# Optimization experiments

Hardware: AMD Instinct MI355X
Metric: run time of the kernel (lower is better)

Reference implementation:

```python
import jax, jax.numpy as jnp
import numpy as np

N_NODES = 100000
N_FEATS = 256
OUT_DIM = 64
NNZ_X = 1280000
N_EDGES = 1600000
KEEP_PROB = 0.9  # 1 - dropout_rate (dropout_rate = 0.1)


def setup_inputs() -> dict:
    key = jax.random.key(0)
    ks = jax.random.split(key, 7)
    feat_values = jax.random.normal(ks[0], (NNZ_X,), dtype=jnp.float32)
    feat_rows = jax.random.randint(ks[1], (NNZ_X,), 0, N_NODES, dtype=jnp.int32)
    feat_cols = jax.random.randint(ks[2], (NNZ_X,), 0, N_FEATS, dtype=jnp.int32)
    # GlorotNormal kernel: std = sqrt(2 / (fan_in + fan_out))
    glorot_std = float(np.sqrt(2.0 / (N_FEATS + OUT_DIM)))
    kernel = jax.random.normal(ks[3], (N_FEATS, OUT_DIM), dtype=jnp.float32) * glorot_std
    adj_values = jax.random.uniform(ks[4], (N_EDGES,), dtype=jnp.float32)
    adj_rows = jax.random.randint(ks[5], (N_EDGES,), 0, N_NODES, dtype=jnp.int32)
    adj_cols = jax.random.randint(ks[6], (N_EDGES,), 0, N_NODES, dtype=jnp.int32)
    return {
        "feat_values": feat_values,
        "kernel": kernel,
        "adj_values": adj_values,
        "feat_rows": feat_rows,
        "feat_cols": feat_cols,
        "adj_rows": adj_rows,
        "adj_cols": adj_cols,
    }


def reference(feat_values, kernel, adj_values, feat_rows, feat_cols, adj_rows, adj_cols):
    # sparse dropout on feature values (training=True path), deterministic key.
    # tf: keep = floor(keep_prob + U[0,1)) cast to bool; retain then scale 1/keep_prob
    u = jax.random.uniform(jax.random.key(42), feat_values.shape, dtype=feat_values.dtype)
    keep = jnp.floor(KEEP_PROB + u).astype(bool)
    v = jnp.where(keep, feat_values, jnp.zeros_like(feat_values)) * (1.0 / KEEP_PROB)

    # SpMM 1: XW[n, o] = sum_{(n,f) in X} v * kernel[f, o]
    xw = jax.ops.segment_sum(v[:, None] * kernel[feat_cols], feat_rows,
                             num_segments=N_NODES)  # [N, OUT]

    # SpMM 2: out[i, o] = sum_{(i,j) in A} a_ij * xw[j, o]
    agg = jax.ops.segment_sum(adj_values[:, None] * xw[adj_cols], adj_rows,
                              num_segments=N_NODES)  # [N, OUT]

    return jax.nn.relu(agg)
```

## Files before the change

kernel.cpp:

```cpp
#include <hip/hip_runtime.h>

#define N_NODES 100000
#define N_FEATS 256
#define OUT_DIM 64
#define NNZ_X   1280000
#define N_EDGES 1600000
#define NB      391
#define CHUNK   4096
#define KPT     8
#define CAPX    4352
#define CAPA    5120

__device__ __forceinline__ unsigned rotl32(unsigned x, unsigned d) {
    return (x << d) | (x >> (32u - d));
}

__device__ __forceinline__ float jax_uniform_42(unsigned e) {
    unsigned x0 = 0u, x1 = e;
    const unsigned ks0 = 0u, ks1 = 42u, ks2 = 0u ^ 42u ^ 0x1BD11BDAu;
    x0 += ks0; x1 += ks1;
#define TF_R(r) { x0 += x1; x1 = rotl32(x1, r); x1 ^= x0; }
    TF_R(13) TF_R(15) TF_R(26) TF_R(6)
    x0 += ks1; x1 += ks2 + 1u;
    TF_R(17) TF_R(29) TF_R(16) TF_R(24)
    x0 += ks2; x1 += ks0 + 2u;
    TF_R(13) TF_R(15) TF_R(26) TF_R(6)
    x0 += ks0; x1 += ks1 + 3u;
    TF_R(17) TF_R(29) TF_R(16) TF_R(24)
    x0 += ks1; x1 += ks2 + 4u;
    TF_R(13) TF_R(15) TF_R(26) TF_R(6)
    x0 += ks2; x1 += ks0 + 5u;
#undef TF_R
    unsigned bits = x0 ^ x1;
    return __uint_as_float((bits >> 9) | 0x3f800000u) - 1.0f;
}

__device__ __forceinline__ bool keep_42(unsigned e) {
    float u = jax_uniform_42(e);
    return floorf(0.9f + u) != 0.0f;
}

__global__ __launch_bounds__(512) void phase1(
        const float* __restrict__ fvals, const int* __restrict__ frows,
        const int* __restrict__ fcols,
        const float* __restrict__ avals, const int* __restrict__ arows,
        const int* __restrict__ acols,
        int* __restrict__ bcur_x, int* __restrict__ bcur_a,
        float2* __restrict__ gx, float2* __restrict__ ga) {
    const int isA = blockIdx.y;
    const float* vals = isA ? avals : fvals;
    const int* rows   = isA ? arows : frows;
    const int* cols   = isA ? acols : fcols;
    int* bcur         = isA ? bcur_a : bcur_x;
    float2* dst       = isA ? ga : gx;
    const unsigned cap = isA ? CAPA : CAPX;
    const unsigned n  = isA ? N_EDGES : NNZ_X;

    unsigned t = threadIdx.x;
    unsigned base = blockIdx.x * CHUNK;
    if (base >= n) return;

    __shared__ int cnt[512];
    __shared__ int start[512];
    __shared__ int cur[512];
    __shared__ int gbase[NB];
    __shared__ int s[256];
    __shared__ unsigned pArr[CHUNK];

    int rcache[KPT];

    cnt[t] = 0;
    __syncthreads();
    #pragma unroll
    for (int k = 0; k < KPT; k++) {
        unsigned i = base + k * 512u + t;
        int r = -1;
        if (i < n) {
            int rr = rows[i];
            if (isA || keep_42(i)) r = rr;
        }
        rcache[k] = r;
        if (r >= 0) atomicAdd(&cnt[(unsigned)r >> 8], 1);
    }
    __syncthreads();
    if (t < 256) s[t] = cnt[2*t] + cnt[2*t+1];
    __syncthreads();
    for (int off = 1; off < 256; off <<= 1) {
        int v = (t < 256u && t >= (unsigned)off) ? s[t - off] : 0;
        __syncthreads();
        if (t < 256u) s[t] += v;
        __syncthreads();
    }
    if (t < 256u) {
        int excl = t ? s[t-1] : 0;
        start[2*t]   = excl;
        start[2*t+1] = excl + cnt[2*t];
        cur[2*t]     = excl;
        cur[2*t+1]   = excl + cnt[2*t];
    }
    for (unsigned b = t; b < NB; b += 512u) {
        int cb = cnt[b];
        if (cb > 0) gbase[b] = atomicAdd(&bcur[b], cb);
    }
    __syncthreads();
    int n_valid = s[255];
    #pragma unroll
    for (int k = 0; k < KPT; k++) {
        int r = rcache[k];
        if (r >= 0) {
            unsigned b = (unsigned)r >> 8;
            int p = atomicAdd(&cur[b], 1);
            pArr[p] = (b << 20) | (((unsigned)r & 255u) << 12) | (k * 512u + t);
        }
    }
    __syncthreads();
    #pragma unroll
    for (int k = 0; k < KPT; k++) {
        int sidx = k * 512 + (int)t;
        if (sidx < n_valid) {
            unsigned m = pArr[sidx];
            unsigned b = m >> 20;
            unsigned rowlow = (m >> 12) & 255u;
            unsigned i = base + (m & 4095u);
            float v = vals[i];
            if (!isA) v *= (float)(1.0 / 0.9);
            unsigned packed = ((unsigned)cols[i] << 8) | rowlow;
            float2 e; e.x = v; e.y = __int_as_float((int)packed);
            dst[(size_t)b * cap + gbase[b] + (sidx - start[b])] = e;
        }
    }
}

__global__ __launch_bounds__(512) void sort_stage(
        const int* __restrict__ bcur_x, const float2* __restrict__ gx,
        const float* __restrict__ W, unsigned short* __restrict__ xw,
        const int* __restrict__ bcur_a, float2* __restrict__ ga,
        unsigned short* __restrict__ rs) {
    __shared__ float2 ent[CAPA];
    __shared__ int hist[256];
    __shared__ int starts[256];
    __shared__ int cursor[256];
    unsigned t = threadIdx.x;
    const int isA = (blockIdx.x >= NB);
    unsigned b = isA ? (blockIdx.x - NB) : blockIdx.x;

    if (!isA) {
        int cnt = bcur_x[b];
        const float2* src = gx + (size_t)b * CAPX;
        if (t < 256) hist[t] = 0;
        __syncthreads();
        for (int i = (int)t; i < cnt; i += 512)
            atomicAdd(&hist[((unsigned)__float_as_int(src[i].y)) & 255u], 1);
        __syncthreads();
        if (t < 256) {
            for (int off = 1; off < 256; off <<= 1) {
                int v = (t >= (unsigned)off) ? hist[t - off] : 0;
                __syncthreads();
                hist[t] += v;
                __syncthreads();
            }
            int excl = t ? hist[t - 1] : 0;
            starts[t] = excl;
            cursor[t] = excl;
        } else {
            for (int off = 1; off < 256; off <<= 1) { __syncthreads(); __syncthreads(); }
        }
        __syncthreads();
        for (int i = (int)t; i < cnt; i += 512) {
            float2 e = src[i];
            int pos = atomicAdd(&cursor[((unsigned)__float_as_int(e.y)) & 255u], 1);
            ent[pos] = e;
        }
        __syncthreads();
        unsigned wid = t >> 6, lane = t & 63u;
        for (unsigned r = wid; r < 256u; r += 8u) {
            int s0 = starts[r];
            int s1 = (r == 255u) ? cnt : starts[r + 1];
            float a[8];
            #pragma unroll
            for (int j = 0; j < 8; j++) a[j] = 0.0f;
            int p = s0;
            for (; p + 8 <= s1; p += 8) {
                float2 e[8];
                #pragma unroll
                for (int j = 0; j < 8; j++) e[j] = ent[p + j];
                float w[8];
                #pragma unroll
                for (int j = 0; j < 8; j++)
                    w[j] = W[(((unsigned)__float_as_int(e[j].y)) >> 8) * OUT_DIM + lane];
                #pragma unroll
                for (int j = 0; j < 8; j++) a[j] = fmaf(e[j].x, w[j], a[j]);
            }
            for (; p < s1; p++) {
                float2 e = ent[p];
                a[0] = fmaf(e.x, W[(((unsigned)__float_as_int(e.y)) >> 8) * OUT_DIM + lane], a[0]);
            }
            unsigned grow = (b << 8) + r;
            if (grow < N_NODES) {
                float acc = ((a[0] + a[1]) + (a[2] + a[3])) + ((a[4] + a[5]) + (a[6] + a[7]));
                unsigned bits = __float_as_uint(acc);
                unsigned rounded = (bits + 0x7fffu + ((bits >> 16) & 1u)) >> 16;
                xw[(size_t)grow * OUT_DIM + lane] = (unsigned short)rounded;
            }
        }
    } else {
        int cnt = bcur_a[b];
        float2* g = ga + (size_t)b * CAPA;
        if (t < 256) hist[t] = 0;
        __syncthreads();
        for (int i = (int)t; i < cnt; i += 512) {
            float2 e = g[i];
            ent[i] = e;
            atomicAdd(&hist[((unsigned)__float_as_int(e.y)) & 255u], 1);
        }
        __syncthreads();
        if (t < 256) {
            for (int off = 1; off < 256; off <<= 1) {
                int v = (t >= (unsigned)off) ? hist[t - off] : 0;
                __syncthreads();
                hist[t] += v;
                __syncthreads();
            }
            int excl = t ? hist[t - 1] : 0;
            cursor[t] = excl;
            rs[(b << 8) + t] = (unsigned short)excl;
        } else {
            for (int off = 1; off < 256; off <<= 1) { __syncthreads(); __syncthreads(); }
        }
        __syncthreads();
        for (int i = (int)t; i < cnt; i += 512) {
            float2 e = ent[i];
            unsigned packed = (unsigned)__float_as_int(e.y);
            int pos = atomicAdd(&cursor[packed & 255u], 1);
            float2 o; o.x = e.x; o.y = __int_as_float((int)(packed >> 8));
            g[pos] = o;
        }
    }
}

__global__ void spmm2(const int* __restrict__ bcur_a,
                      const unsigned short* __restrict__ rs_a,
                      const float2* __restrict__ ga,
                      const unsigned short* __restrict__ xw,
                      float* __restrict__ out) {
    unsigned row  = blockIdx.x * 4u + (threadIdx.x >> 6);
    unsigned lane = threadIdx.x & 63u;
    if (row >= N_NODES) return;
    unsigned b = row >> 8, rl = row & 255u;
    int cnt = bcur_a[b];
    const float2* ent = ga + (size_t)b * CAPA;
    int s0 = rs_a[row];
    int s1 = (rl == 255u) ? cnt : (int)rs_a[row + 1];
    unsigned half = lane >> 5;
    unsigned sub  = lane & 31u;
    const ushort2* xw2 = (const ushort2*)xw;

    float2 acc[4];
    #pragma unroll
    for (int j = 0; j < 4; j++) { acc[j].x = 0.0f; acc[j].y = 0.0f; }
    int p = s0;
    for (; p + 8 <= s1; p += 8) {
        float2 e[4];
        #pragma unroll
        for (int j = 0; j < 4; j++) e[j] = ent[p + 4 * half + j];
        ushort2 u[4];
        #pragma unroll
        for (int j = 0; j < 4; j++)
            u[j] = xw2[((unsigned)__float_as_int(e[j].y)) * 32u + sub];
        #pragma unroll
        for (int j = 0; j < 4; j++) {
            float xx = __uint_as_float((unsigned)u[j].x << 16);
            float xy = __uint_as_float((unsigned)u[j].y << 16);
            acc[j].x = fmaf(e[j].x, xx, acc[j].x);
            acc[j].y = fmaf(e[j].x, xy, acc[j].y);
        }
    }
    for (int q = p + (int)half; q < s1; q += 2) {
        float2 e = ent[q];
        ushort2 u = xw2[((unsigned)__float_as_int(e.y)) * 32u + sub];
        acc[0].x = fmaf(e.x, __uint_as_float((unsigned)u.x << 16), acc[0].x);
        acc[0].y = fmaf(e.x, __uint_as_float((unsigned)u.y << 16), acc[0].y);
    }
    float ax = (acc[0].x + acc[1].x) + (acc[2].x + acc[3].x);
    float ay = (acc[0].y + acc[1].y) + (acc[2].y + acc[3].y);
    ax += __shfl(ax, (int)(lane ^ 32u), 64);
    ay += __shfl(ay, (int)(lane ^ 32u), 64);
    if (half == 0) {
        float2 o;
        o.x = fmaxf(ax, 0.0f);
        o.y = fmaxf(ay, 0.0f);
        ((float2*)out)[(size_t)row * 32u + sub] = o;
    }
}

extern "C" void kernel_launch(void* const* d_in, const int* in_sizes, int n_in,
                              void* d_out, int out_size, void* d_ws, size_t ws_size,
                              hipStream_t stream) {
    const float* feat_values = (const float*)d_in[0];
    const float* W           = (const float*)d_in[1];
    const float* adj_values  = (const float*)d_in[2];
    const int*   feat_rows   = (const int*)d_in[3];
    const int*   feat_cols   = (const int*)d_in[4];
    const int*   adj_rows    = (const int*)d_in[5];
    const int*   adj_cols    = (const int*)d_in[6];
    float* out = (float*)d_out;

    char* ws = (char*)d_ws;
    int* bcur_x = (int*)(ws + 0);
    int* bcur_a = (int*)(ws + 2048);
    unsigned short* rs_a = (unsigned short*)(ws + 4096);
    float2* gx  = (float2*)(ws + 204800);
    float2* ga  = (float2*)(ws + 13817856);
    unsigned short* xw = (unsigned short*)(ws + 29833216);

    hipMemsetAsync(ws, 0, 4096, stream);

    dim3 gp1((N_EDGES + CHUNK - 1) / CHUNK, 2);
    phase1<<<gp1, 512, 0, stream>>>(feat_values, feat_rows, feat_cols,
                                    adj_values, adj_rows, adj_cols,
                                    bcur_x, bcur_a, gx, ga);
    sort_stage<<<2 * NB, 512, 0, stream>>>(bcur_x, gx, W, xw, bcur_a, ga, rs_a);
    spmm2<<<(N_NODES + 3) / 4, 256, 0, stream>>>(bcur_a, rs_a, ga, xw, out);
}
```

Baseline: 223.1 us.

## Use wavefront shuffle scans and half-wave float2 SpMM in sort stage

Replaces the 256-thread Hillis-Steele scan, which used shared memory and 16 barriers, with a per-wavefront __shfl_up scan combined through four wave totals, cutting block-wide synchronisation. The feature-row SpMM now has each half-wave process alternate entries with float2 loads of W and a shuffle reduction. The adjacency path keeps entries in registers (10 per thread) instead of staging them in shared memory, which lets the shared buffer shrink to CAPX and may raise occupancy. The trade-off is higher register pressure and a hard cap of 5120 entries per bucket in the register path.

```diff
diff --git a/kernel.cpp b/kernel.cpp
--- a/kernel.cpp
+++ b/kernel.cpp
@@ -40,6 +40,11 @@
     return floorf(0.9f + u) != 0.0f;
 }
 
+__device__ __forceinline__ unsigned short f32_bf16(float f) {
+    unsigned bits = __float_as_uint(f);
+    return (unsigned short)((bits + 0x7fffu + ((bits >> 16) & 1u)) >> 16);
+}
+
 __global__ __launch_bounds__(512) void phase1(
         const float* __restrict__ fvals, const int* __restrict__ frows,
         const int* __restrict__ fcols,
@@ -136,11 +141,13 @@
         const float* __restrict__ W, unsigned short* __restrict__ xw,
         const int* __restrict__ bcur_a, float2* __restrict__ ga,
         unsigned short* __restrict__ rs) {
-    __shared__ float2 ent[CAPA];
+    __shared__ float2 ent[CAPX];
     __shared__ int hist[256];
     __shared__ int starts[256];
     __shared__ int cursor[256];
+    __shared__ int wtot[4];
     unsigned t = threadIdx.x;
+    unsigned wid = t >> 6, lane = t & 63u;
     const int isA = (blockIdx.x >= NB);
     unsigned b = isA ? (blockIdx.x - NB) : blockIdx.x;
 
@@ -152,18 +159,27 @@
         for (int i = (int)t; i < cnt; i += 512)
             atomicAdd(&hist[((unsigned)__float_as_int(src[i].y)) & 255u], 1);
         __syncthreads();
-        if (t < 256) {
-            for (int off = 1; off < 256; off <<= 1) {
-                int v = (t >= (unsigned)off) ? hist[t - off] : 0;
-                __syncthreads();
-                hist[t] += v;
-                __syncthreads();
-            }
-            int excl = t ? hist[t - 1] : 0;
-            starts[t] = excl;
-            cursor[t] = excl;
-        } else {
-            for (int off = 1; off < 256; off <<= 1) { __syncthreads(); __syncthreads(); }
+        int inc = 0, binv = 0;
+        if (wid < 4u) {
+            unsigned bin = wid * 64u + lane;
+            binv = hist[bin];
+            inc = binv;
+            #pragma unroll
+            for (int d = 1; d < 64; d <<= 1) {
+                int v = __shfl_up(inc, d, 64);
+                if (lane >= (unsigned)d) inc += v;
+            }
+            if (lane == 63u) wtot[wid] = inc;
+        }
+        __syncthreads();
+        if (wid < 4u) {
+            int offw = 0;
+            #pragma unroll
+            for (int w = 0; w < 4; w++) if ((unsigned)w < wid) offw += wtot[w];
+            unsigned bin = wid * 64u + lane;
+            int excl = inc - binv + offw;
+            starts[bin] = excl;
+            cursor[bin] = excl;
         }
         __syncthreads();
         for (int i = (int)t; i < cnt; i += 512) {
@@ -172,35 +188,44 @@
             ent[pos] = e;
         }
         __syncthreads();
-        unsigned wid = t >> 6, lane = t & 63u;
+        unsigned half = lane >> 5, sub = lane & 31u;
+        const float2* W2 = (const float2*)W;
+        ushort2* xw2 = (ushort2*)xw;
         for (unsigned r = wid; r < 256u; r += 8u) {
             int s0 = starts[r];
             int s1 = (r == 255u) ? cnt : starts[r + 1];
-            float a[8];
-            #pragma unroll
-            for (int j = 0; j < 8; j++) a[j] = 0.0f;
+            float2 acc[4];
+            #pragma unroll
+            for (int j = 0; j < 4; j++) { acc[j].x = 0.0f; acc[j].y = 0.0f; }
             int p = s0;
             for (; p + 8 <= s1; p += 8) {
-                float2 e[8];
+                float2 e[4];
                 #pragma unroll
-                for (int j = 0; j < 8; j++) e[j] = ent[p + j];
-                float w[8];
+                for (int j = 0; j < 4; j++) e[j] = ent[p + 4 * half + j];
+                float2 w[4];
                 #pragma unroll
-                for (int j = 0; j < 8; j++)
-                    w[j] = W[(((unsigned)__float_as_int(e[j].y)) >> 8) * OUT_DIM + lane];
+                for (int j = 0; j < 4; j++)
+                    w[j] = W2[(((unsigned)__float_as_int(e[j].y)) >> 8) * 32u + sub];
                 #pragma unroll
-                for (int j = 0; j < 8; j++) a[j] = fmaf(e[j].x, w[j], a[j]);
-            }
-            for (; p < s1; p++) {
-                float2 e = ent[p];
-                a[0] = fmaf(e.x, W[(((unsigned)__float_as_int(e.y)) >> 8) * OUT_DIM + lane], a[0]);
-            }
+                for (int j = 0; j < 4; j++) {
+                    acc[j].x = fmaf(e[j].x, w[j].x, acc[j].x);
+                    acc[j].y = fmaf(e[j].x, w[j].y, acc[j].y);
+                }
+            }
+            for (int q = p + (int)half; q < s1; q += 2) {
+                float2 e = ent[q];
+                float2 w = W2[(((unsigned)__float_as_int(e.y)) >> 8) * 32u + sub];
+                acc[0].x = fmaf(e.x, w.x, acc[0].x);
+                acc[0].y = fmaf(e.x, w.y, acc[0].y);
+            }
+            float ax = (acc[0].x + acc[1].x) + (acc[2].x + acc[3].x);
+            float ay = (acc[0].y + acc[1].y) + (acc[2].y + acc[3].y);
+            ax += __shfl(ax, (int)(lane ^ 32u), 64);
+            ay += __shfl(ay, (int)(lane ^ 32u), 64);
             unsigned grow = (b << 8) + r;
-            if (grow < N_NODES) {
-                float acc = ((a[0] + a[1]) + (a[2] + a[3])) + ((a[4] + a[5]) + (a[6] + a[7]));
-                unsigned bits = __float_as_uint(acc);
-                unsigned rounded = (bits + 0x7fffu + ((bits >> 16) & 1u)) >> 16;
-                xw[(size_t)grow * OUT_DIM + lane] = (unsigned short)rounded;
+            if (half == 0 && grow < N_NODES) {
+                ushort2 o; o.x = f32_bf16(ax); o.y = f32_bf16(ay);
+                xw2[(size_t)grow * 32u + sub] = o;
             }
         }
     } else {
@@ -208,32 +233,49 @@
         float2* g = ga + (size_t)b * CAPA;
         if (t < 256) hist[t] = 0;
         __syncthreads();
-        for (int i = (int)t; i < cnt; i += 512) {
-            float2 e = g[i];
-            ent[i] = e;
-            atomicAdd(&hist[((unsigned)__float_as_int(e.y)) & 255u], 1);
-        }
-        __syncthreads();
-        if (t < 256) {
-            for (int off = 1; off < 256; off <<= 1) {
-                int v = (t >= (unsigned)off) ? hist[t - off] : 0;
-                __syncthreads();
-                hist[t] += v;
-                __syncthreads();
-            }
-            int excl = t ? hist[t - 1] : 0;
-            cursor[t] = excl;
-            rs[(b << 8) + t] = (unsigned short)excl;
-        } else {
-            for (int off = 1; off < 256; off <<= 1) { __syncthreads(); __syncthreads(); }
-        }
-        __syncthreads();
-        for (int i = (int)t; i < cnt; i += 512) {
-            float2 e = ent[i];
-            unsigned packed = (unsigned)__float_as_int(e.y);
-            int pos = atomicAdd(&cursor[packed & 255u], 1);
-            float2 o; o.x = e.x; o.y = __int_as_float((int)(packed >> 8));
-            g[pos] = o;
+        float2 ec[10];
+        #pragma unroll
+        for (int k = 0; k < 10; k++) {
+            int i = k * 512 + (int)t;
+            if (i < cnt) {
+                float2 e = g[i];
+                ec[k] = e;
+                atomicAdd(&hist[((unsigned)__float_as_int(e.y)) & 255u], 1);
+            }
+        }
+        __syncthreads();
+        int inc = 0, binv = 0;
+        if (wid < 4u) {
+            unsigned bin = wid * 64u + lane;
+            binv = hist[bin];
+            inc = binv;
+            #pragma unroll
+            for (int d = 1; d < 64; d <<= 1) {
+                int v = __shfl_up(inc, d, 64);
+                if (lane >= (unsigned)d) inc += v;
+            }
+            if (lane == 63u) wtot[wid] = inc;
+        }
+        __syncthreads();
+        if (wid < 4u) {
+            int offw = 0;
+            #pragma unroll
+            for (int w = 0; w < 4; w++) if ((unsigned)w < wid) offw += wtot[w];
+            unsigned bin = wid * 64u + lane;
+            int excl = inc - binv + offw;
+            cursor[bin] = excl;
+            rs[(b << 8) + bin] = (unsigned short)excl;
+        }
+        __syncthreads();
+        #pragma unroll
+        for (int k = 0; k < 10; k++) {
+            int i = k * 512 + (int)t;
+            if (i < cnt) {
+                unsigned packed = (unsigned)__float_as_int(ec[k].y);
+                int pos = atomicAdd(&cursor[packed & 255u], 1);
+                float2 o; o.x = ec[k].x; o.y = __int_as_float((int)(packed >> 8));
+                g[pos] = o;
+            }
         }
     }
 }
```

After: 215.5 us. 3.4% less time.
